# Performance work log

Measured on AMD Instinct MI355X. Metric: run time of the kernel, lower is better.

## Reference

```python
import jax, jax.numpy as jnp
import numpy as np

T, DY, DP, DIN, H = 96, 90, 80, 170, 4096
WEI_Y, WEI_P = 1.0, 1.0  # wei_Y, wei_P diagonal objective weights


def setup_inputs() -> dict:
    key = jax.random.key(0)
    ks = jax.random.split(key, 20)
    s = 0.02
    return {
        "J_tr_en": jax.random.normal(ks[0], (T, DIN), jnp.float32),
        "P_price": jax.random.uniform(ks[1], (T, DP), jnp.float32),
        "Upp_Y": jax.random.uniform(ks[2], (T, DY), jnp.float32) + 0.5,
        "Low_Y": jax.random.uniform(ks[3], (T, DY), jnp.float32) - 0.5,
        "Upp_P": jax.random.uniform(ks[4], (T, DP), jnp.float32) + 0.5,
        "Low_P": jax.random.uniform(ks[5], (T, DP), jnp.float32) - 0.5,
        # pretrained FNN weights (m_state_dict): 170 -> 4096 -> 4096 -> 4096 -> 90
        "W1": jax.random.normal(ks[6], (DIN, H), jnp.float32) * s,
        "b1": jnp.zeros((H,), jnp.float32),
        "W2": jax.random.normal(ks[7], (H, H), jnp.float32) * s,
        "b2": jnp.zeros((H,), jnp.float32),
        "W3": jax.random.normal(ks[8], (H, H), jnp.float32) * s,
        "b3": jnp.zeros((H,), jnp.float32),
        "W4": jax.random.normal(ks[9], (H, DY), jnp.float32) * s,
        "b4": jnp.zeros((DY,), jnp.float32),
        # scalers: scale = SS_max - SS_min, min = SS_min (diagonal matmul + row-constant bias)
        "scale_Y": jax.random.uniform(ks[10], (DY,), jnp.float32) + 0.5,
        "min_Y": jax.random.uniform(ks[11], (DY,), jnp.float32) - 0.5,
        "scale_P": jax.random.uniform(ks[12], (DP,), jnp.float32) + 0.5,
        "min_P": jax.random.uniform(ks[13], (DP,), jnp.float32) - 0.5,
    }


def reference(J_tr_en, P_price, Upp_Y, Low_Y, Upp_P, Low_P,
              W1, b1, W2, b2, W3, b3, W4, b4,
              scale_Y, min_Y, scale_P, min_P):
    def mlp(x):  # x: [170]
        h = jax.nn.relu(x @ W1 + b1)
        h = jax.nn.relu(h @ W2 + b2)
        h = jax.nn.relu(h @ W3 + b3)
        return h @ W4 + b4  # [90]

    u_tail = J_tr_en[:-1, DY:]      # [95, 80] exogenous tail per step
    y0 = J_tr_en[0, :DY]            # [90]

    def step(y, ut):
        out = mlp(jnp.concatenate([y, ut]))
        return out, out

    _, ys = jax.lax.scan(step, y0, u_tail)
    u_y = jnp.concatenate([y0[None, :], ys], axis=0)  # [96, 90]

    # diagonal 'linear' layers == elementwise scale + bias
    Yhy = u_y * scale_Y + min_Y                        # [96, 90]
    Phy = J_tr_en[:, DY:DIN] * scale_P + min_P         # [96, 80]

    # sum_Y_weight / sum_P_weight are identity matrices -> no-op matmuls
    Obj_Y_upp = jax.nn.relu(WEI_Y * Yhy - Upp_Y)
    Obj_Y_low = jax.nn.relu(-WEI_Y * Yhy + Low_Y)
    Obj_P_1 = Phy * P_price
    Obj_P_2upp = jax.nn.relu(WEI_P * Phy - Upp_P)
    Obj_P_2low = jax.nn.relu(-WEI_P * Phy + Low_P)
    return (Obj_Y_upp, Obj_Y_low, Obj_P_1, Obj_P_2upp, Obj_P_2low)
```

## Files before the change

### kernel.cpp

```cpp
#include <hip/hip_runtime.h>

#define NB 256
#define BLK 1024
#define TSn 95
#define DYn 90
#define DPn 80
#define DINn 170
#define Hn 4096

typedef unsigned int uint32;
typedef unsigned long long uint64;
typedef _Float16 h2v __attribute__((ext_vector_type(2)));

#define B_W3T 0ull
#define B_MT  33554432ull
#define B_UPB 67108864ull
#define B_C   67887104ull
#define B_H1X 67903488ull
#define B_H2X 67919872ull
#define B_H3X 67936256ull
#define B_H3H 67952640ull
#define WS_NEED 68730880ull

#define O_YU 0
#define O_YL 8640
#define O_P1 17280
#define O_PU 24960
#define O_PL 32640

__device__ __forceinline__ void st_tag(uint64* p, uint64 v) {
  __hip_atomic_store(p, v, __ATOMIC_RELAXED, __HIP_MEMORY_SCOPE_AGENT);
}
__device__ __forceinline__ uint64 ld_tag(const uint64* p) {
  return __hip_atomic_load(p, __ATOMIC_RELAXED, __HIP_MEMORY_SCOPE_AGENT);
}
__device__ __forceinline__ uint32 pkh(float x, float y) {
  h2v h; h[0] = (_Float16)x; h[1] = (_Float16)y;
  return __builtin_bit_cast(uint32, h);
}
__device__ __forceinline__ float hlo(uint32 u) { h2v h = __builtin_bit_cast(h2v, u); return (float)h[0]; }
__device__ __forceinline__ float hhi(uint32 u) { h2v h = __builtin_bit_cast(h2v, u); return (float)h[1]; }
__device__ __forceinline__ float dot2(uint32 a, uint32 b, float c) {
  return __builtin_amdgcn_fdot2(__builtin_bit_cast(h2v, a), __builtin_bit_cast(h2v, b), c, false);
}
__device__ __forceinline__ float wred(float v) {
#pragma unroll
  for (int o = 32; o > 0; o >>= 1) v += __shfl_xor(v, o, 64);
  return v;
}

extern "C" __global__ __launch_bounds__(256)
void t3_kernel(const float* __restrict__ W3, uint32* __restrict__ W3T) {
  const int m = blockIdx.x;
  const int j0 = (m >> 6) * 64, k0 = (m & 63) * 64;
  const int t = threadIdx.x;
  __shared__ float lds[64][65];
  const int jl = t & 63, kb = t >> 6;
#pragma unroll
  for (int i = 0; i < 16; ++i) {
    const int kl = kb + 4 * i;
    lds[kl][jl] = W3[(size_t)(k0 + kl) * Hn + j0 + jl];
  }
  __syncthreads();
  const int kp = t & 31, jb = t >> 5;
#pragma unroll
  for (int i = 0; i < 8; ++i) {
    const int jr = jb + 8 * i;
    W3T[(size_t)(j0 + jr) * 2048 + (k0 >> 1) + kp] = pkh(lds[2 * kp][jr], lds[2 * kp + 1][jr]);
  }
}

extern "C" __global__ __launch_bounds__(256)
void m_kernel(const float* __restrict__ W1, const float* __restrict__ W4,
              uint32* __restrict__ MT) {
  const int j0 = (blockIdx.x >> 6) * 64, k0 = (blockIdx.x & 63) * 64;
  const int tid = threadIdx.x;
  __shared__ __align__(16) float aW[90][64];
  __shared__ __align__(16) float bT[90][64];
  for (int i = tid; i < 90 * 64; i += 256) {
    const int q = i >> 6, jl = i & 63;
    aW[q][jl] = W1[(size_t)q * Hn + j0 + jl];
  }
  for (int i = tid; i < 90 * 64; i += 256) {
    const int q = i >> 6, kl = i & 63;
    bT[q][kl] = W4[(size_t)(k0 + kl) * DYn + q];
  }
  __syncthreads();
  const int ty = tid >> 4, tx = tid & 15;
  float acc[4][4] = {};
#pragma unroll 2
  for (int q = 0; q < DYn; ++q) {
    const float4 av = *(const float4*)&aW[q][ty * 4];
    const float4 bv = *(const float4*)&bT[q][tx * 4];
    const float ar[4] = {av.x, av.y, av.z, av.w};
    const float br[4] = {bv.x, bv.y, bv.z, bv.w};
#pragma unroll
    for (int r = 0; r < 4; ++r)
#pragma unroll
      for (int c = 0; c < 4; ++c) acc[r][c] = fmaf(ar[r], br[c], acc[r][c]);
  }
#pragma unroll
  for (int r = 0; r < 4; ++r) {
    const size_t row = (size_t)(j0 + ty * 4 + r) * 2048 + (k0 >> 1) + tx * 2;
#pragma unroll
    for (int c = 0; c < 2; ++c)
      MT[row + c] = pkh(acc[r][2 * c], acc[r][2 * c + 1]);
  }
}

extern "C" __global__ __launch_bounds__(256)
void c_kernel(const float* __restrict__ W1, const float* __restrict__ b4,
              float* __restrict__ c) {
  const int j = blockIdx.x * 256 + threadIdx.x;
  float a = 0.f;
#pragma unroll 6
  for (int q = 0; q < DYn; ++q) a = fmaf(b4[q], W1[(size_t)q * Hn + j], a);
  c[j] = a;
}

extern "C" __global__ __launch_bounds__(512)
void up_kernel(const float* __restrict__ J, const float* __restrict__ W1,
               const float* __restrict__ b1, uint32* __restrict__ UPb) {
  const int t = blockIdx.x >> 3, jc = blockIdx.x & 7;
  const int j = jc * 512 + threadIdx.x;
  __shared__ float us[DPn];
  __shared__ float oa[512];
  if (threadIdx.x < DPn) us[threadIdx.x] = J[(size_t)t * DINn + DYn + threadIdx.x];
  __syncthreads();
  float acc = b1[j];
#pragma unroll 8
  for (int k = 0; k < DPn; ++k) acc = fmaf(us[k], W1[(size_t)(DYn + k) * Hn + j], acc);
  oa[threadIdx.x] = acc;
  __syncthreads();
  if (threadIdx.x < 256)
    UPb[(size_t)t * 2048 + jc * 256 + threadIdx.x] = pkh(oa[2 * threadIdx.x], oa[2 * threadIdx.x + 1]);
}

__device__ __forceinline__ float dot_lds(const uint32* __restrict__ Wrow,
                                         const uint32* __restrict__ hvp, int l) {
  float a = 0.f;
#pragma unroll
  for (int i = 0; i < 8; ++i) {
    const uint4 u = *(const uint4*)&Wrow[i * 256 + l * 4];
    const uint4 h = *(const uint4*)&hvp[i * 256 + l * 4];
    a = dot2(h.x, u.x, a); a = dot2(h.y, u.y, a);
    a = dot2(h.z, u.z, a); a = dot2(h.w, u.w, a);
  }
  return wred(a);
}

__device__ __forceinline__ float dot_pf(const uint4* pf, const uint32* __restrict__ hvp, int l) {
  float a = 0.f;
#pragma unroll
  for (int i = 0; i < 8; ++i) {
    const uint4 h = *(const uint4*)&hvp[i * 256 + l * 4];
    const uint4 u = pf[i];
    a = dot2(h.x, u.x, a); a = dot2(h.y, u.y, a);
    a = dot2(h.z, u.z, a); a = dot2(h.w, u.w, a);
  }
  return wred(a);
}

__device__ __forceinline__ void pull_h(const uint64* __restrict__ X, uint32* __restrict__ hvp,
                                       uint32 tag, int tid) {
  uint64 v0 = ld_tag(X + tid);
  uint64 v1 = ld_tag(X + tid + 1024);
  unsigned spins = 0;
  while ((uint32)(v0 >> 32) != tag || (uint32)(v1 >> 32) != tag) {
    __builtin_amdgcn_s_sleep(1);
    if ((uint32)(v0 >> 32) != tag) v0 = ld_tag(X + tid);
    if ((uint32)(v1 >> 32) != tag) v1 = ld_tag(X + tid + 1024);
    if (++spins > (1u << 22)) break;
  }
  hvp[tid] = (uint32)v0;
  hvp[tid + 1024] = (uint32)v1;
}

extern "C" __global__ __launch_bounds__(BLK, 1)
void scan10_kernel(const float* __restrict__ J, const float* __restrict__ b2,
                   const float* __restrict__ b3, const float* __restrict__ W1,
                   const float* __restrict__ W2, const uint32* __restrict__ W3T,
                   const uint32* __restrict__ MT, const uint32* __restrict__ UPb,
                   const float* __restrict__ cv,
                   uint64* __restrict__ H1X, uint64* __restrict__ H2X,
                   uint64* __restrict__ H3X, uint32* __restrict__ H3H) {
  const int bid = blockIdx.x, tid = threadIdx.x;
  const int w = tid >> 6, l = tid & 63;
  const int j0 = bid * 16, j = j0 + w;

  __shared__ __align__(16) uint32 W2L[16 * 2048];
  __shared__ __align__(16) uint32 hvp[2048];
  __shared__ float h1s[16];
  __shared__ float ysA[96];

  for (int kp = tid; kp < 2048; kp += BLK) {
    const float* r0 = W2 + (size_t)(2 * kp) * Hn + j0;
    const float* r1 = r0 + Hn;
#pragma unroll
    for (int q = 0; q < 4; ++q) {
      const float4 a4 = *(const float4*)(r0 + 4 * q);
      const float4 c4 = *(const float4*)(r1 + 4 * q);
      W2L[(4 * q + 0) * 2048 + kp] = pkh(a4.x, c4.x);
      W2L[(4 * q + 1) * 2048 + kp] = pkh(a4.y, c4.y);
      W2L[(4 * q + 2) * 2048 + kp] = pkh(a4.z, c4.z);
      W2L[(4 * q + 3) * 2048 + kp] = pkh(a4.w, c4.w);
    }
  }
  uint4 pf[8];
  __syncthreads();

  for (int t = 0; t < TSn; ++t) {
    if (t == 0) {
      if (tid < DYn) ysA[tid] = J[tid];
      __syncthreads();
      float a = 0.f;
      if (l < DYn) a = ysA[l] * W1[(size_t)l * Hn + j];
      if (l + 64 < DYn) a = fmaf(ysA[l + 64], W1[(size_t)(l + 64) * Hn + j], a);
      a = wred(a);
      if (l == 0) {
        const uint32 uu = UPb[(j >> 1)];
        h1s[w] = fmaxf(((j & 1) ? hhi(uu) : hlo(uu)) + a, 0.f);
      }
    } else {
      pull_h(H3X, hvp, (uint32)t, tid);
      __syncthreads();
      const float a = dot_pf(pf, hvp, l);
      if (l == 0) {
        const uint32 uu = UPb[(size_t)t * 2048 + (j >> 1)];
        h1s[w] = fmaxf(((j & 1) ? hhi(uu) : hlo(uu)) + cv[j] + a, 0.f);
      }
    }
    __syncthreads();
    if (tid < 8) {
      const uint32 pk = pkh(h1s[2 * tid], h1s[2 * tid + 1]);
      st_tag(H1X + bid * 8 + tid, (uint64)pk | ((uint64)(t + 1) << 32));
    }

    {
      const uint4* wr = (const uint4*)W3T + (size_t)j * 512 + l;
#pragma unroll
      for (int i = 0; i < 8; ++i) pf[i] = wr[i * 64];
    }

    pull_h(H1X, hvp, (uint32)(t + 1), tid);
    __syncthreads();
    {
      const float a = dot_lds(&W2L[w * 2048], hvp, l);
      if (l == 0) h1s[w] = fmaxf(b2[j] + a, 0.f);
    }
    __syncthreads();
    if (tid < 8) {
      const uint32 pk = pkh(h1s[2 * tid], h1s[2 * tid + 1]);
      st_tag(H2X + bid * 8 + tid, (uint64)pk | ((uint64)(t + 1) << 32));
    }

    pull_h(H2X, hvp, (uint32)(t + 1), tid);
    __syncthreads();
    {
      const float a = dot_pf(pf, hvp, l);
      if (l == 0) h1s[w] = fmaxf(b3[j] + a, 0.f);
    }
    __syncthreads();
    if (tid < 8) {
      const uint32 pk = pkh(h1s[2 * tid], h1s[2 * tid + 1]);
      st_tag(H3X + bid * 8 + tid, (uint64)pk | ((uint64)(t + 1) << 32));
      H3H[(size_t)t * 2048 + bid * 8 + tid] = pk;
    }

    {
      const uint4* wr = (const uint4*)MT + (size_t)j * 512 + l;
#pragma unroll
      for (int i = 0; i < 8; ++i) pf[i] = wr[i * 64];
    }
  }
}

extern "C" __global__ __launch_bounds__(1024)
void post2_kernel(const float* __restrict__ J, const float* __restrict__ Pp,
                  const float* __restrict__ UppY, const float* __restrict__ LowY,
                  const float* __restrict__ UppP, const float* __restrict__ LowP,
                  const float* __restrict__ W4, const float* __restrict__ b4,
                  const float* __restrict__ scY, const float* __restrict__ mnY,
                  const float* __restrict__ scP, const float* __restrict__ mnP,
                  const uint32* __restrict__ H3H, float* __restrict__ out) {
  const int t = blockIdx.x, tid = threadIdx.x;
  __shared__ float h3s[4096];
  __shared__ float ps[8][128];
  __shared__ float ysv[96];
  if (t > 0) {
    for (int i = tid; i < 2048; i += 1024) {
      const uint32 u = H3H[(size_t)(t - 1) * 2048 + i];
      h3s[2 * i] = hlo(u);
      h3s[2 * i + 1] = hhi(u);
    }
    __syncthreads();
    const int p = tid >> 7, d = tid & 127;
    if (d < DYn) {
      float a = 0.f;
      const float* wp = W4 + d;
      const int k0 = p * 512;
#pragma unroll 8
      for (int k = k0; k < k0 + 512; ++k) a = fmaf(h3s[k], wp[(size_t)k * DYn], a);
      ps[p][d] = a;
    }
    __syncthreads();
    if (tid < DYn) {
      float s = b4[tid];
#pragma unroll
      for (int p2 = 0; p2 < 8; ++p2) s += ps[p2][tid];
      ysv[tid] = s;
    }
  } else {
    if (tid < DYn) ysv[tid] = J[tid];
  }
  __syncthreads();
  if (tid < DPn) {
    const float ph = fmaf(J[(size_t)t * DINn + DYn + tid], scP[tid], mnP[tid]);
    out[O_P1 + t * DPn + tid] = ph * Pp[t * DPn + tid];
    out[O_PU + t * DPn + tid] = fmaxf(ph - UppP[t * DPn + tid], 0.f);
    out[O_PL + t * DPn + tid] = fmaxf(LowP[t * DPn + tid] - ph, 0.f);
  }
  if (tid < DYn) {
    const float yh = fmaf(ysv[tid], scY[tid], mnY[tid]);
    out[O_YU + t * DYn + tid] = fmaxf(yh - UppY[t * DYn + tid], 0.f);
    out[O_YL + t * DYn + tid] = fmaxf(LowY[t * DYn + tid] - yh, 0.f);
  }
}

extern "C" void kernel_launch(void* const* d_in, const int* in_sizes, int n_in,
                              void* d_out, int out_size, void* d_ws, size_t ws_size,
                              hipStream_t stream) {
  const float* J    = (const float*)d_in[0];
  const float* Pp   = (const float*)d_in[1];
  const float* UppY = (const float*)d_in[2];
  const float* LowY = (const float*)d_in[3];
  const float* UppP = (const float*)d_in[4];
  const float* LowP = (const float*)d_in[5];
  const float* W1   = (const float*)d_in[6];
  const float* b1   = (const float*)d_in[7];
  const float* W2   = (const float*)d_in[8];
  const float* b2   = (const float*)d_in[9];
  const float* W3   = (const float*)d_in[10];
  const float* b3   = (const float*)d_in[11];
  const float* W4   = (const float*)d_in[12];
  const float* b4   = (const float*)d_in[13];
  const float* scY  = (const float*)d_in[14];
  const float* mnY  = (const float*)d_in[15];
  const float* scP  = (const float*)d_in[16];
  const float* mnP  = (const float*)d_in[17];
  float* out = (float*)d_out;

  if (ws_size < WS_NEED) return;

  char* base = (char*)d_ws;
  uint32* W3T = (uint32*)(base + B_W3T);
  uint32* MT  = (uint32*)(base + B_MT);
  uint32* UPb = (uint32*)(base + B_UPB);
  float*  cv  = (float*)(base + B_C);
  uint64* H1X = (uint64*)(base + B_H1X);
  uint64* H2X = (uint64*)(base + B_H2X);
  uint64* H3X = (uint64*)(base + B_H3X);
  uint32* H3H = (uint32*)(base + B_H3H);

  t3_kernel<<<dim3(4096), dim3(256), 0, stream>>>(W3, W3T);
  m_kernel<<<dim3(4096), dim3(256), 0, stream>>>(W1, W4, MT);
  c_kernel<<<dim3(16), dim3(256), 0, stream>>>(W1, b4, cv);
  up_kernel<<<dim3(TSn * 8), dim3(512), 0, stream>>>(J, W1, b1, UPb);
  scan10_kernel<<<dim3(NB), dim3(BLK), 0, stream>>>(
      J, b2, b3, W1, W2, W3T, MT, UPb, cv, H1X, H2X, H3X, H3H);
  post2_kernel<<<dim3(96), dim3(1024), 0, stream>>>(
      J, Pp, UppY, LowY, UppP, LowP, W4, b4, scY, mnY, scP, mnP, H3H, out);
}
```

Before: 817.9 us.

## Merge prep kernels into one launch and use packed fp16 W4 in post kernel

Folds the four preprocessing kernels (W3 transpose, W1·W4 product, bias vector, exogenous-input projection) into a single block-indexed prep_kernel, which saves three launches and lets the independent jobs run side by side. It also adds a packed half-precision copy of W4 (pairs of rows interleaved, padded to 96 columns), so the post kernel can use dot2 on packed H3 values and stop converting them to fp32 in LDS. This costs extra workspace and a little more fp16 rounding in the final layer.

```diff
diff --git a/kernel.cpp b/kernel.cpp
--- a/kernel.cpp
+++ b/kernel.cpp
@@ -20,7 +20,8 @@
 #define B_H2X 67919872ull
 #define B_H3X 67936256ull
 #define B_H3H 67952640ull
-#define WS_NEED 68730880ull
+#define B_W4T 68730880ull
+#define WS_NEED 69517312ull
 
 #define O_YU 0
 #define O_YL 8640
@@ -49,91 +50,105 @@
   return v;
 }
 
+#define G_T3 4096
+#define G_M  8192
+#define G_C  8208
+#define G_UP 9728
+#define G_W4 9920
+
 extern "C" __global__ __launch_bounds__(256)
-void t3_kernel(const float* __restrict__ W3, uint32* __restrict__ W3T) {
-  const int m = blockIdx.x;
-  const int j0 = (m >> 6) * 64, k0 = (m & 63) * 64;
-  const int t = threadIdx.x;
-  __shared__ float lds[64][65];
-  const int jl = t & 63, kb = t >> 6;
-#pragma unroll
-  for (int i = 0; i < 16; ++i) {
-    const int kl = kb + 4 * i;
-    lds[kl][jl] = W3[(size_t)(k0 + kl) * Hn + j0 + jl];
-  }
-  __syncthreads();
-  const int kp = t & 31, jb = t >> 5;
-#pragma unroll
-  for (int i = 0; i < 8; ++i) {
-    const int jr = jb + 8 * i;
-    W3T[(size_t)(j0 + jr) * 2048 + (k0 >> 1) + kp] = pkh(lds[2 * kp][jr], lds[2 * kp + 1][jr]);
-  }
-}
-
-extern "C" __global__ __launch_bounds__(256)
-void m_kernel(const float* __restrict__ W1, const float* __restrict__ W4,
-              uint32* __restrict__ MT) {
-  const int j0 = (blockIdx.x >> 6) * 64, k0 = (blockIdx.x & 63) * 64;
-  const int tid = threadIdx.x;
-  __shared__ __align__(16) float aW[90][64];
-  __shared__ __align__(16) float bT[90][64];
-  for (int i = tid; i < 90 * 64; i += 256) {
-    const int q = i >> 6, jl = i & 63;
-    aW[q][jl] = W1[(size_t)q * Hn + j0 + jl];
-  }
-  for (int i = tid; i < 90 * 64; i += 256) {
-    const int q = i >> 6, kl = i & 63;
-    bT[q][kl] = W4[(size_t)(k0 + kl) * DYn + q];
-  }
-  __syncthreads();
-  const int ty = tid >> 4, tx = tid & 15;
-  float acc[4][4] = {};
+void prep_kernel(const float* __restrict__ J, const float* __restrict__ W1,
+                 const float* __restrict__ b1, const float* __restrict__ W3,
+                 const float* __restrict__ W4, const float* __restrict__ b4,
+                 uint32* __restrict__ W3T, uint32* __restrict__ MT,
+                 float* __restrict__ cv, uint32* __restrict__ UPb,
+                 uint32* __restrict__ W4T2) {
+  const int b = blockIdx.x, tid = threadIdx.x;
+
+  if (b < G_T3) {
+    const int j0 = (b >> 6) * 64, k0 = (b & 63) * 64;
+    __shared__ float lds[64][65];
+    const int jl = tid & 63, kb = tid >> 6;
+#pragma unroll
+    for (int i = 0; i < 16; ++i) {
+      const int kl = kb + 4 * i;
+      lds[kl][jl] = W3[(size_t)(k0 + kl) * Hn + j0 + jl];
+    }
+    __syncthreads();
+    const int kp = tid & 31, jb = tid >> 5;
+#pragma unroll
+    for (int i = 0; i < 8; ++i) {
+      const int jr = jb + 8 * i;
+      W3T[(size_t)(j0 + jr) * 2048 + (k0 >> 1) + kp] = pkh(lds[2 * kp][jr], lds[2 * kp + 1][jr]);
+    }
+  } else if (b < G_M) {
+    const int mb = b - G_T3;
+    const int j0 = (mb >> 6) * 64, k0 = (mb & 63) * 64;
+    __shared__ __align__(16) float aW[90][64];
+    __shared__ __align__(16) float bT[90][64];
+    for (int i = tid; i < 90 * 64; i += 256) {
+      const int q = i >> 6, jl = i & 63;
+      aW[q][jl] = W1[(size_t)q * Hn + j0 + jl];
+    }
+    for (int i = tid; i < 90 * 64; i += 256) {
+      const int q = i >> 6, kl = i & 63;
+      bT[q][kl] = W4[(size_t)(k0 + kl) * DYn + q];
+    }
+    __syncthreads();
+    const int ty = tid >> 4, tx = tid & 15;
+    float acc[4][4] = {};
 #pragma unroll 2
-  for (int q = 0; q < DYn; ++q) {
-    const float4 av = *(const float4*)&aW[q][ty * 4];
-    const float4 bv = *(const float4*)&bT[q][tx * 4];
-    const float ar[4] = {av.x, av.y, av.z, av.w};
-    const float br[4] = {bv.x, bv.y, bv.z, bv.w};
-#pragma unroll
-    for (int r = 0; r < 4; ++r)
-#pragma unroll
-      for (int c = 0; c < 4; ++c) acc[r][c] = fmaf(ar[r], br[c], acc[r][c]);
-  }
-#pragma unroll
-  for (int r = 0; r < 4; ++r) {
-    const size_t row = (size_t)(j0 + ty * 4 + r) * 2048 + (k0 >> 1) + tx * 2;
-#pragma unroll
-    for (int c = 0; c < 2; ++c)
-      MT[row + c] = pkh(acc[r][2 * c], acc[r][2 * c + 1]);
-  }
-}
-
-extern "C" __global__ __launch_bounds__(256)
-void c_kernel(const float* __restrict__ W1, const float* __restrict__ b4,
-              float* __restrict__ c) {
-  const int j = blockIdx.x * 256 + threadIdx.x;
-  float a = 0.f;
+    for (int q = 0; q < DYn; ++q) {
+      const float4 av = *(const float4*)&aW[q][ty * 4];
+      const float4 bv = *(const float4*)&bT[q][tx * 4];
+      const float ar[4] = {av.x, av.y, av.z, av.w};
+      const float br[4] = {bv.x, bv.y, bv.z, bv.w};
+#pragma unroll
+      for (int r = 0; r < 4; ++r)
+#pragma unroll
+        for (int c = 0; c < 4; ++c) acc[r][c] = fmaf(ar[r], br[c], acc[r][c]);
+    }
+#pragma unroll
+    for (int r = 0; r < 4; ++r) {
+      const size_t row = (size_t)(j0 + ty * 4 + r) * 2048 + (k0 >> 1) + tx * 2;
+#pragma unroll
+      for (int c = 0; c < 2; ++c)
+        MT[row + c] = pkh(acc[r][2 * c], acc[r][2 * c + 1]);
+    }
+  } else if (b < G_C) {
+    const int j = (b - G_M) * 256 + tid;
+    float a = 0.f;
 #pragma unroll 6
-  for (int q = 0; q < DYn; ++q) a = fmaf(b4[q], W1[(size_t)q * Hn + j], a);
-  c[j] = a;
-}
-
-extern "C" __global__ __launch_bounds__(512)
-void up_kernel(const float* __restrict__ J, const float* __restrict__ W1,
-               const float* __restrict__ b1, uint32* __restrict__ UPb) {
-  const int t = blockIdx.x >> 3, jc = blockIdx.x & 7;
-  const int j = jc * 512 + threadIdx.x;
-  __shared__ float us[DPn];
-  __shared__ float oa[512];
-  if (threadIdx.x < DPn) us[threadIdx.x] = J[(size_t)t * DINn + DYn + threadIdx.x];
-  __syncthreads();
-  float acc = b1[j];
+    for (int q = 0; q < DYn; ++q) a = fmaf(b4[q], W1[(size_t)q * Hn + j], a);
+    cv[j] = a;
+  } else if (b < G_UP) {
+    const int bb = b - G_C;
+    const int t = bb >> 4, jc = bb & 15;
+    const int j = jc * 256 + tid;
+    __shared__ float us[DPn];
+    __shared__ float oa[256];
+    if (tid < DPn) us[tid] = J[(size_t)t * DINn + DYn + tid];
+    __syncthreads();
+    float acc = b1[j];
 #pragma unroll 8
-  for (int k = 0; k < DPn; ++k) acc = fmaf(us[k], W1[(size_t)(DYn + k) * Hn + j], acc);
-  oa[threadIdx.x] = acc;
-  __syncthreads();
-  if (threadIdx.x < 256)
-    UPb[(size_t)t * 2048 + jc * 256 + threadIdx.x] = pkh(oa[2 * threadIdx.x], oa[2 * threadIdx.x + 1]);
+    for (int k = 0; k < DPn; ++k) acc = fmaf(us[k], W1[(size_t)(DYn + k) * Hn + j], acc);
+    oa[tid] = acc;
+    __syncthreads();
+    if (tid < 128)
+      UPb[(size_t)t * 2048 + jc * 128 + tid] = pkh(oa[2 * tid], oa[2 * tid + 1]);
+  } else {
+    const int bb = b - G_UP;
+    for (int k = 0; k < 4; ++k) {
+      const int idx = (bb * 256 + tid) + k * 49152;
+      const int i = idx / 96, d = idx - i * 96;
+      float v0 = 0.f, v1 = 0.f;
+      if (d < DYn) {
+        v0 = W4[(size_t)(2 * i) * DYn + d];
+        v1 = W4[(size_t)(2 * i + 1) * DYn + d];
+      }
+      W4T2[(size_t)i * 96 + d] = pkh(v0, v1);
+    }
+  }
 }
 
 __device__ __forceinline__ float dot_lds(const uint32* __restrict__ Wrow,
@@ -276,31 +291,27 @@
 }
 
 extern "C" __global__ __launch_bounds__(1024)
-void post2_kernel(const float* __restrict__ J, const float* __restrict__ Pp,
+void post3_kernel(const float* __restrict__ J, const float* __restrict__ Pp,
                   const float* __restrict__ UppY, const float* __restrict__ LowY,
                   const float* __restrict__ UppP, const float* __restrict__ LowP,
-                  const float* __restrict__ W4, const float* __restrict__ b4,
+                  const uint32* __restrict__ W4T2, const float* __restrict__ b4,
                   const float* __restrict__ scY, const float* __restrict__ mnY,
                   const float* __restrict__ scP, const float* __restrict__ mnP,
                   const uint32* __restrict__ H3H, float* __restrict__ out) {
   const int t = blockIdx.x, tid = threadIdx.x;
-  __shared__ float h3s[4096];
+  __shared__ uint32 h3p[2048];
   __shared__ float ps[8][128];
   __shared__ float ysv[96];
   if (t > 0) {
-    for (int i = tid; i < 2048; i += 1024) {
-      const uint32 u = H3H[(size_t)(t - 1) * 2048 + i];
-      h3s[2 * i] = hlo(u);
-      h3s[2 * i + 1] = hhi(u);
-    }
+    for (int i = tid; i < 2048; i += 1024) h3p[i] = H3H[(size_t)(t - 1) * 2048 + i];
     __syncthreads();
     const int p = tid >> 7, d = tid & 127;
-    if (d < DYn) {
+    if (d < 96) {
       float a = 0.f;
-      const float* wp = W4 + d;
-      const int k0 = p * 512;
+      const uint32* wr = W4T2 + (size_t)(p * 256) * 96 + d;
+      const uint32* hp = h3p + p * 256;
 #pragma unroll 8
-      for (int k = k0; k < k0 + 512; ++k) a = fmaf(h3s[k], wp[(size_t)k * DYn], a);
+      for (int i = 0; i < 256; ++i) a = dot2(hp[i], wr[(size_t)i * 96], a);
       ps[p][d] = a;
     }
     __syncthreads();
@@ -353,21 +364,20 @@
   if (ws_size < WS_NEED) return;
 
   char* base = (char*)d_ws;
-  uint32* W3T = (uint32*)(base + B_W3T);
-  uint32* MT  = (uint32*)(base + B_MT);
-  uint32* UPb = (uint32*)(base + B_UPB);
-  float*  cv  = (float*)(base + B_C);
-  uint64* H1X = (uint64*)(base + B_H1X);
-  uint64* H2X = (uint64*)(base + B_H2X);
-  uint64* H3X = (uint64*)(base + B_H3X);
-  uint32* H3H = (uint32*)(base + B_H3H);
-
-  t3_kernel<<<dim3(4096), dim3(256), 0, stream>>>(W3, W3T);
-  m_kernel<<<dim3(4096), dim3(256), 0, stream>>>(W1, W4, MT);
-  c_kernel<<<dim3(16), dim3(256), 0, stream>>>(W1, b4, cv);
-  up_kernel<<<dim3(TSn * 8), dim3(512), 0, stream>>>(J, W1, b1, UPb);
+  uint32* W3T  = (uint32*)(base + B_W3T);
+  uint32* MT   = (uint32*)(base + B_MT);
+  uint32* UPb  = (uint32*)(base + B_UPB);
+  float*  cv   = (float*)(base + B_C);
+  uint64* H1X  = (uint64*)(base + B_H1X);
+  uint64* H2X  = (uint64*)(base + B_H2X);
+  uint64* H3X  = (uint64*)(base + B_H3X);
+  uint32* H3H  = (uint32*)(base + B_H3H);
+  uint32* W4T2 = (uint32*)(base + B_W4T);
+
+  prep_kernel<<<dim3(G_W4), dim3(256), 0, stream>>>(
+      J, W1, b1, W3, W4, b4, W3T, MT, cv, UPb, W4T2);
   scan10_kernel<<<dim3(NB), dim3(BLK), 0, stream>>>(
       J, b2, b3, W1, W2, W3T, MT, UPb, cv, H1X, H2X, H3X, H3H);
-  post2_kernel<<<dim3(96), dim3(1024), 0, stream>>>(
-      J, Pp, UppY, LowY, UppP, LowP, W4, b4, scY, mnY, scP, mnP, H3H, out);
-}
+  post3_kernel<<<dim3(96), dim3(1024), 0, stream>>>(
+      J, Pp, UppY, LowY, UppP, LowP, W4T2, b4, scY, mnY, scP, mnP, H3H, out);
+}
```

Measured after the change: 811.5 us. Within noise of the previous version (-0.8%).
